# Kernel optimization log

Measured on AMD Instinct MI355X. Metric: run time of the kernel, lower is better.

Reference implementation:

```python
import jax, jax.numpy as jnp
import numpy as np

N, E = 50000, 1600000
DIM_IN, DIM_H, HEADS, DIM_OUT, EDGE_DIM = 64, 16, 8, 64, 1
HID = DIM_H * HEADS  # 128


def setup_inputs() -> dict:
    key = jax.random.key(0)
    ks = jax.random.split(key, 20)
    s = 0.1
    return {
        "x": jax.random.normal(ks[0], (N, DIM_IN), jnp.float32),
        "edge_index": jax.random.randint(ks[1], (2, E), 0, N, jnp.int32),
        "edge_weight": jax.random.uniform(ks[2], (E, EDGE_DIM), jnp.float32),
        # gat1 params (GATv2Conv: lin_l, lin_r with bias, lin_edge no bias, att, out bias)
        "w1_l": jax.random.normal(ks[3], (DIM_IN, HID), jnp.float32) * s,
        "b1_l": jnp.zeros((HID,), jnp.float32),
        "w1_r": jax.random.normal(ks[4], (DIM_IN, HID), jnp.float32) * s,
        "b1_r": jnp.zeros((HID,), jnp.float32),
        "w1_e": jax.random.normal(ks[5], (EDGE_DIM, HID), jnp.float32) * s,
        "att1": jax.random.normal(ks[6], (HEADS, DIM_H), jnp.float32) * s,
        "bias1": jnp.zeros((HID,), jnp.float32),
        # gat2 params (heads=1)
        "w2_l": jax.random.normal(ks[7], (HID, DIM_OUT), jnp.float32) * s,
        "b2_l": jnp.zeros((DIM_OUT,), jnp.float32),
        "w2_r": jax.random.normal(ks[8], (HID, DIM_OUT), jnp.float32) * s,
        "b2_r": jnp.zeros((DIM_OUT,), jnp.float32),
        "w2_e": jax.random.normal(ks[9], (EDGE_DIM, DIM_OUT), jnp.float32) * s,
        "att2": jax.random.normal(ks[10], (1, DIM_OUT), jnp.float32) * s,
        "bias2": jnp.zeros((DIM_OUT,), jnp.float32),
        # final fc
        "fc_w": jax.random.normal(ks[11], (DIM_OUT, 1), jnp.float32) * s,
        "fc_b": jnp.zeros((1,), jnp.float32),
    }


def _gatv2(x, src, dst, eattr, wl, bl, wr, br, we, att, bias, H, C):
    n = x.shape[0]
    xl = (x @ wl + bl).reshape(n, H, C)
    xr = (x @ wr + br).reshape(n, H, C)
    e = (eattr @ we).reshape(-1, H, C)
    # GATv2: score on summed, leaky-relu'd features (edge-wise)
    m = jax.nn.leaky_relu(xl[src] + xr[dst] + e, 0.2)  # [Etot, H, C]
    logits = jnp.einsum('ehc,hc->eh', m, att)
    lmax = jax.ops.segment_max(logits, dst, num_segments=n)
    ex = jnp.exp(logits - lmax[dst])
    denom = jax.ops.segment_sum(ex, dst, num_segments=n)
    alpha = ex / denom[dst]  # segment softmax over neighborhoods
    out = jax.ops.segment_sum(alpha[:, :, None] * xl[src], dst, num_segments=n)
    return out.reshape(n, H * C) + bias


def reference(x, edge_index, edge_weight,
              w1_l, b1_l, w1_r, b1_r, w1_e, att1, bias1,
              w2_l, b2_l, w2_r, b2_r, w2_e, att2, bias2,
              fc_w, fc_b):
    n = x.shape[0]
    src, dst = edge_index[0], edge_index[1]
    # add self-loops with edge_attr fill_value='mean' (PyG default)
    ones = jnp.ones((src.shape[0], 1), x.dtype)
    cnt = jax.ops.segment_sum(ones, dst, num_segments=n)
    sm = jax.ops.segment_sum(edge_weight, dst, num_segments=n)
    mean_attr = jnp.where(cnt > 0, sm / jnp.maximum(cnt, 1.0), 0.0)
    loop = jnp.arange(n, dtype=src.dtype)
    src_f = jnp.concatenate([src, loop])
    dst_f = jnp.concatenate([dst, loop])
    eattr = jnp.concatenate([edge_weight, mean_attr], axis=0)

    # dropout(p=0.6) is identity in eval mode
    h = _gatv2(x, src_f, dst_f, eattr, w1_l, b1_l, w1_r, b1_r, w1_e, att1, bias1, HEADS, DIM_H)
    h = jax.nn.elu(h)
    h = _gatv2(h, src_f, dst_f, eattr, w2_l, b2_l, w2_r, b2_r, w2_e, att2, bias2, 1, DIM_OUT)
    h = jax.nn.log_softmax(h, axis=1)
    return h @ fc_w + fc_b  # [N, 1]
```

## Files before the change

### kernel.cpp

```cpp
#include <hip/hip_runtime.h>
#include <hip/hip_fp16.h>

#define HEADS 8
#define HID 128
#define DIN 64
#define DOUT 64
#define NBLK 512
#define BSH 8
#define BS 256
#define MAXNB 512

typedef _Float16 f16x2 __attribute__((ext_vector_type(2)));
union U8 { uint4 u4[2]; f16x2 h[8]; };
union X8 { uint4 u4[8]; f16x2 h[32]; };

__device__ __forceinline__ int h2i(f16x2 h) { union { f16x2 h; int i; } u; u.h = h; return u.i; }
__device__ __forceinline__ f16x2 i2h(int i) { union { f16x2 h; int i; } u; u.i = i; return u.h; }
__device__ __forceinline__ _Float16 us2h(unsigned short v) { union { unsigned short u; _Float16 h; } u; u.u = v; return u.h; }

__device__ __forceinline__ void cvt16(const uint4 v, f16x2* o) {
#if __has_builtin(__builtin_amdgcn_cvt_scalef32_pk_f16_fp8)
    o[0] = __builtin_amdgcn_cvt_scalef32_pk_f16_fp8(v.x, 1.0f, false);
    o[1] = __builtin_amdgcn_cvt_scalef32_pk_f16_fp8(v.x, 1.0f, true);
    o[2] = __builtin_amdgcn_cvt_scalef32_pk_f16_fp8(v.y, 1.0f, false);
    o[3] = __builtin_amdgcn_cvt_scalef32_pk_f16_fp8(v.y, 1.0f, true);
    o[4] = __builtin_amdgcn_cvt_scalef32_pk_f16_fp8(v.z, 1.0f, false);
    o[5] = __builtin_amdgcn_cvt_scalef32_pk_f16_fp8(v.z, 1.0f, true);
    o[6] = __builtin_amdgcn_cvt_scalef32_pk_f16_fp8(v.w, 1.0f, false);
    o[7] = __builtin_amdgcn_cvt_scalef32_pk_f16_fp8(v.w, 1.0f, true);
#else
    const f16x2 s256 = (f16x2){(_Float16)256.f, (_Float16)256.f};
    const unsigned* uu = &v.x;
#pragma unroll
    for (int j = 0; j < 4; ++j) {
        unsigned u = uu[j];
        unsigned plo = u & 0xFFFFu, phi = u >> 16;
        unsigned flo = ((plo & 0x80u) << 8) | ((plo & 0x7Fu) << 7)
                     | ((plo & 0x8000u) << 16) | ((plo & 0x7F00u) << 15);
        unsigned fhi = ((phi & 0x80u) << 8) | ((phi & 0x7Fu) << 7)
                     | ((phi & 0x8000u) << 16) | ((phi & 0x7F00u) << 15);
        o[2*j]   = i2h((int)flo) * s256;
        o[2*j+1] = i2h((int)fhi) * s256;
    }
#endif
}

__device__ __forceinline__ unsigned enc_fp8(float a) {
    float c = fminf(fmaxf(a, -448.f), 448.f);
    unsigned short hb = __half_as_ushort(__float2half(c));
    unsigned s = ((unsigned)hb >> 8) & 0x80u;
    unsigned lsb = (hb >> 7) & 1u;
    unsigned hr = (unsigned)hb + 0x3Fu + lsb;
    int e = (int)((hr >> 10) & 0x1Fu);
    if (e <= 8) {
        int m8 = (int)rintf(fabsf(c) * 512.f);
        if (m8 >= 8) return s | (1u << 3);
        return s | (unsigned)m8;
    }
    unsigned m3 = (hr >> 7) & 7u;
    int ef = e - 8;
    if (ef > 15) { ef = 15; m3 = 7u; }
    return s | ((unsigned)ef << 3) | m3;
}

__device__ __forceinline__ unsigned char to_fp8(float a) {
#if __has_builtin(__builtin_amdgcn_cvt_pk_fp8_f32)
    int v = __builtin_amdgcn_cvt_pk_fp8_f32(a, a, 0, false);
    return (unsigned char)(v & 0xFF);
#else
    return (unsigned char)enc_fp8(a);
#endif
}

__global__ void k_hist(const int* __restrict__ ei, int* __restrict__ h, int E, int NB) {
    __shared__ int hist[MAXNB];
    int i = blockIdx.x, t = threadIdx.x;
    for (int b = t; b < NB; b += 256) hist[b] = 0;
    __syncthreads();
    int chunk = (E + NBLK - 1) / NBLK;
    int e0 = i * chunk, e1 = min(E, e0 + chunk);
    for (int e = e0 + t; e < e1; e += 256) {
        int d = ei[E + e];
        atomicAdd(&hist[d >> BSH], 1);
    }
    __syncthreads();
    for (int b = t; b < NB; b += 256) h[b * NBLK + i] = hist[b];
}

__global__ void k_scancol(int* __restrict__ h, int* __restrict__ Btot, int NB) {
    __shared__ int s[256];
    int b = blockIdx.x, t = threadIdx.x;
    int* col = h + (size_t)b * NBLK;
    int v0 = col[2 * t], v1 = col[2 * t + 1];
    int pair = v0 + v1;
    s[t] = pair;
    __syncthreads();
    for (int off = 1; off < 256; off <<= 1) {
        int u = (t >= off) ? s[t - off] : 0;
        __syncthreads();
        s[t] += u;
        __syncthreads();
    }
    int excl = s[t] - pair;
    col[2 * t] = excl;
    col[2 * t + 1] = excl + v0;
    if (t == 255) Btot[b] = s[255];
}

__global__ void k_scanbuck(const int* __restrict__ Btot, int* __restrict__ Boff,
                           int* __restrict__ rowptr, int E, int N, int NB) {
    __shared__ int s[256];
    int t = threadIdx.x;
    int v = (t < NB) ? Btot[t] : 0;
    s[t] = v;
    __syncthreads();
    for (int off = 1; off < 256; off <<= 1) {
        int u = (t >= off) ? s[t - off] : 0;
        __syncthreads();
        s[t] += u;
        __syncthreads();
    }
    if (t < NB) Boff[t] = s[t] - v;
    if (t == 0) { Boff[NB] = E; rowptr[N] = E + N; }
}

__global__ void k_scatter(const int* __restrict__ ei, const float* __restrict__ ew,
                          const int* __restrict__ h, const int* __restrict__ Boff,
                          int2* __restrict__ barr, int E, int NB) {
    __shared__ int base[MAXNB];
    int i = blockIdx.x, t = threadIdx.x;
    for (int b = t; b < NB; b += 256) base[b] = h[b * NBLK + i] + Boff[b];
    __syncthreads();
    int chunk = (E + NBLK - 1) / NBLK;
    int e0 = i * chunk, e1 = min(E, e0 + chunk);
    for (int e = e0 + t; e < e1; e += 256) {
        int s = ei[e], d = ei[E + e];
        float w = ew[e];
        int slot = atomicAdd(&base[d >> BSH], 1);
        barr[slot] = make_int2(((d & (BS - 1)) << 16) | s, __float_as_int(w));
    }
}

__global__ void k_csr(const int2* __restrict__ barr, const int* __restrict__ Boff,
                      int* __restrict__ rowptr, unsigned* __restrict__ csrw, int N, int NB) {
    __shared__ int cnt[BS];
    __shared__ int wfix[BS];
    __shared__ int off[BS];
    __shared__ int fill[BS];
    int b = blockIdx.x, t = threadIdx.x;
    int n0 = b << BSH;
    int nodes = min(BS, N - n0);
    cnt[t] = 0; wfix[t] = 0;
    __syncthreads();
    int j0 = Boff[b], j1 = Boff[b + 1];
    for (int j = j0 + t; j < j1; j += BS) {
        int2 rec = barr[j];
        int dl = rec.x >> 16;
        atomicAdd(&cnt[dl], 1);
        atomicAdd(&wfix[dl], (int)(__int_as_float(rec.y) * 16777216.0f));
    }
    __syncthreads();
    int v = (t < nodes) ? cnt[t] + 1 : 0;
    off[t] = v;
    __syncthreads();
    for (int o = 1; o < BS; o <<= 1) {
        int u = (t >= o) ? off[t - o] : 0;
        __syncthreads();
        off[t] += u;
        __syncthreads();
    }
    int rowBase = j0 + n0;
    int rs = rowBase + off[t] - v;
    if (t < nodes) {
        rowptr[n0 + t] = rs;
        int c = cnt[t];
        float mean = (c > 0) ? ((float)wfix[t] * (1.f / 16777216.f)) / (float)c : 0.f;
        csrw[rs + c] = (unsigned)(n0 + t)
                     | ((unsigned)__half_as_ushort(__float2half(mean)) << 16);
        fill[t] = rs;
    }
    __syncthreads();
    for (int j = j0 + t; j < j1; j += BS) {
        int2 rec = barr[j];
        int dl = rec.x >> 16;
        int pos = atomicAdd(&fill[dl], 1);
        unsigned wb = (unsigned)__half_as_ushort(__float2half(__int_as_float(rec.y)));
        csrw[pos] = (unsigned)(rec.x & 0xFFFF) | (wb << 16);
    }
}

__global__ void k_x16(const float* __restrict__ x, __half* __restrict__ x16, int total8) {
    int i = blockIdx.x * blockDim.x + threadIdx.x;
    if (i >= total8) return;
    const float4* p = (const float4*)(x + (size_t)i * 8);
    float4 a = p[0], b = p[1];
    union { __half h[8]; uint4 u; } o;
    o.h[0] = __float2half(a.x); o.h[1] = __float2half(a.y);
    o.h[2] = __float2half(a.z); o.h[3] = __float2half(a.w);
    o.h[4] = __float2half(b.x); o.h[5] = __float2half(b.y);
    o.h[6] = __float2half(b.z); o.h[7] = __float2half(b.w);
    ((uint4*)x16)[i] = o.u;
}

__global__ __launch_bounds__(256) void k_proj1(
        const __half* __restrict__ x16,
        const float* __restrict__ wl, const float* __restrict__ bl,
        const float* __restrict__ wr, const float* __restrict__ br,
        unsigned char* __restrict__ xl8, __half* __restrict__ xr16, int N) {
    int t = threadIdx.x;
    bool isL = t < 128;
    int j = isL ? t : t - 128;
    const float* w = isL ? wl : wr;
    float bj = isL ? bl[j] : br[j];
    f16x2 wreg[32];
#pragma unroll
    for (int k = 0; k < 32; ++k)
        wreg[k] = (f16x2){(_Float16)w[(2*k) * HID + j], (_Float16)w[(2*k+1) * HID + j]};
    for (int n = blockIdx.x; n < N; n += gridDim.x) {
        X8 xa;
        const uint4* xp = (const uint4*)(x16 + (size_t)n * DIN);
#pragma unroll
        for (int q = 0; q < 8; ++q) xa.u4[q] = xp[q];
        float acc = 0.f;
#pragma unroll
        for (int k = 0; k < 32; ++k) acc = __builtin_amdgcn_fdot2(xa.h[k], wreg[k], acc, false);
        acc += bj;
        if (isL) xl8[(size_t)n * HID + j] = to_fp8(acc);
        else     xr16[(size_t)n * HID + j] = __float2half(acc);
    }
}

__global__ __launch_bounds__(128) void k_proj2(
        const __half* __restrict__ h1,
        const float* __restrict__ wl, const float* __restrict__ bl,
        const float* __restrict__ wr, const float* __restrict__ br,
        unsigned char* __restrict__ xl8, __half* __restrict__ xr16, int N) {
    int t = threadIdx.x;
    bool isL = t < 64;
    int j = isL ? t : t - 64;
    const float* w = isL ? wl : wr;
    float bj = isL ? bl[j] : br[j];
    f16x2 wreg0[32], wreg1[32];
#pragma unroll
    for (int k = 0; k < 32; ++k) {
        wreg0[k] = (f16x2){(_Float16)w[(2*k) * DOUT + j], (_Float16)w[(2*k+1) * DOUT + j]};
        wreg1[k] = (f16x2){(_Float16)w[(64 + 2*k) * DOUT + j], (_Float16)w[(64 + 2*k+1) * DOUT + j]};
    }
    for (int n = blockIdx.x; n < N; n += gridDim.x) {
        const uint4* xp = (const uint4*)(h1 + (size_t)n * HID);
        float acc = 0.f;
        {
            X8 xa;
#pragma unroll
            for (int q = 0; q < 8; ++q) xa.u4[q] = xp[q];
#pragma unroll
            for (int k = 0; k < 32; ++k) acc = __builtin_amdgcn_fdot2(xa.h[k], wreg0[k], acc, false);
        }
        {
            X8 xa;
#pragma unroll
            for (int q = 0; q < 8; ++q) xa.u4[q] = xp[8 + q];
#pragma unroll
            for (int k = 0; k < 32; ++k) acc = __builtin_amdgcn_fdot2(xa.h[k], wreg1[k], acc, false);
        }
        acc += bj;
        if (isL) xl8[(size_t)n * DOUT + j] = to_fp8(acc);
        else     xr16[(size_t)n * DOUT + j] = __float2half(acc);
    }
}

#define G1_FETCH(R, SLOT) \
    rec##R = __shfl(creg, (SLOT) * 8 + es); \
    buf##R = *(const uint4*)(xl8 + ((rec##R & 0xFFFFu) * 128u + (unsigned)cb));

#define G1_COMP(R, SLOT) { \
    f16x2 xv[8]; \
    cvt16(buf##R, xv); \
    bool live = (s0 + (SLOT) * 8 + es) < r1; \
    _Float16 wh = us2h((unsigned short)(rec##R >> 16)); \
    f16x2 w2 = (f16x2){wh, wh}; \
    float p0 = 0.f, p1 = 0.f; \
    _Pragma("unroll") \
    for (int k = 0; k < 8; k += 2) { \
        f16x2 m0 = xv[k] + __builtin_elementwise_fma(w2, we2[k], xr.h[k]); \
        m0 = __builtin_elementwise_max(m0, m0 * c02); \
        p0 = __builtin_amdgcn_fdot2(m0, at2[k], p0, false); \
        f16x2 m1 = xv[k+1] + __builtin_elementwise_fma(w2, we2[k+1], xr.h[k+1]); \
        m1 = __builtin_elementwise_max(m1, m1 * c02); \
        p1 = __builtin_amdgcn_fdot2(m1, at2[k+1], p1, false); \
    } \
    float ex = live ? __expf(p0 + p1) : 0.f; \
    den += ex; \
    _Float16 exh = (_Float16)ex; \
    f16x2 ex2 = (f16x2){exh, exh}; \
    _Pragma("unroll") \
    for (int k = 0; k < 8; ++k) num2[k] = __builtin_elementwise_fma(ex2, xv[k], num2[k]); }

__global__ __launch_bounds__(256) void k_gat1(
        const int* __restrict__ rowptr, const unsigned* __restrict__ csr,
        const unsigned char* __restrict__ xl8, const __half* __restrict__ xr16,
        const float* __restrict__ w1e, const float* __restrict__ att,
        const float* __restrict__ bias, __half* __restrict__ h1,
        int N, int totWaves) {
    int lane = threadIdx.x & 63;
    int wv = (blockIdx.x * blockDim.x + threadIdx.x) >> 6;
    int es = lane & 7, h = lane >> 3;
    int cb = h * 16;
    f16x2 we2[8], at2[8];
#pragma unroll
    for (int k = 0; k < 8; ++k) {
        we2[k] = (f16x2){(_Float16)w1e[cb + 2*k], (_Float16)w1e[cb + 2*k + 1]};
        at2[k] = (f16x2){(_Float16)att[cb + 2*k], (_Float16)att[cb + 2*k + 1]};
    }
    float2 bs = *(const float2*)(bias + cb + es * 2);
    const f16x2 c02 = (f16x2){(_Float16)0.2f, (_Float16)0.2f};

    int r0 = 0, r1 = 0;
    if (wv < N) { r0 = rowptr[wv]; r1 = rowptr[wv + 1]; }
    for (int n = wv; n < N; n += totWaves) {
        int nn = n + totWaves;
        int r0n = 0, r1n = 0;
        if (nn < N) { r0n = rowptr[nn]; r1n = rowptr[nn + 1]; }

        U8 xr;
        { const uint4* p = (const uint4*)(xr16 + (unsigned)(n * HID + cb)); xr.u4[0] = p[0]; xr.u4[1] = p[1]; }
        float den = 0.f;
        f16x2 num2[8];
#pragma unroll
        for (int k = 0; k < 8; ++k) num2[k] = (f16x2){(_Float16)0.f, (_Float16)0.f};

        for (int s0 = r0; s0 < r1; s0 += 64) {
            unsigned creg = csr[min(s0 + lane, r1 - 1)];
            unsigned recA, recB, recC;
            uint4 bufA, bufB, bufC;
            G1_FETCH(A, 0)
            G1_FETCH(B, 1)
            G1_FETCH(C, 2)
            G1_COMP(A, 0)
            if (s0 + 24 < r1) { G1_FETCH(A, 3) }
            if (s0 + 8 < r1) {
                G1_COMP(B, 1)
                if (s0 + 32 < r1) { G1_FETCH(B, 4) }
                if (s0 + 16 < r1) {
                    G1_COMP(C, 2)
                    if (s0 + 40 < r1) { G1_FETCH(C, 5) }
                    if (s0 + 24 < r1) {
                        G1_COMP(A, 3)
                        if (s0 + 48 < r1) { G1_FETCH(A, 6) }
                        if (s0 + 32 < r1) {
                            G1_COMP(B, 4)
                            if (s0 + 56 < r1) { G1_FETCH(B, 7) }
                            if (s0 + 40 < r1) {
                                G1_COMP(C, 5)
                                if (s0 + 48 < r1) {
                                    G1_COMP(A, 6)
                                    if (s0 + 56 < r1) {
                                        G1_COMP(B, 7)
                                    }
                                }
                            }
                        }
                    }
                }
            }
        }
        den += __shfl_xor(den, 1); den += __shfl_xor(den, 2); den += __shfl_xor(den, 4);
        bool h4 = es & 4, h2 = es & 2, h1b = es & 1;
        f16x2 r4[4];
#pragma unroll
        for (int k = 0; k < 4; ++k) {
            f16x2 send_ = h4 ? num2[k] : num2[k + 4];
            f16x2 recv = i2h(__shfl_xor(h2i(send_), 4));
            r4[k] = (h4 ? num2[k + 4] : num2[k]) + recv;
        }
        f16x2 r2[2];
#pragma unroll
        for (int k = 0; k < 2; ++k) {
            f16x2 send_ = h2 ? r4[k] : r4[k + 2];
            f16x2 recv = i2h(__shfl_xor(h2i(send_), 2));
            r2[k] = (h2 ? r4[k + 2] : r4[k]) + recv;
        }
        f16x2 send_ = h1b ? r2[0] : r2[1];
        f16x2 recv = i2h(__shfl_xor(h2i(send_), 1));
        f16x2 rfin = (h1b ? r2[1] : r2[0]) + recv;

        float inv = 1.f / den;
        float v0 = fmaf((float)rfin[0], inv, bs.x);
        float v1 = fmaf((float)rfin[1], inv, bs.y);
        v0 = v0 > 0.f ? v0 : expm1f(v0);
        v1 = v1 > 0.f ? v1 : expm1f(v1);
        *(__half2*)(h1 + (unsigned)(n * HID + cb + es * 2)) = __floats2half2_rn(v0, v1);
        r0 = r0n; r1 = r1n;
    }
}

#define G2_FETCH(R, SLOT) \
    rec##R = __shfl(creg, (SLOT) * 16 + es); \
    buf##R = *(const uint4*)(xl8 + ((rec##R & 0xFFFFu) * 64u + (unsigned)cb));

#define G2_COMP(R, SLOT) { \
    f16x2 xv[8]; \
    cvt16(buf##R, xv); \
    bool live = (s0 + (SLOT) * 16 + es) < r1; \
    _Float16 wh = us2h((unsigned short)(rec##R >> 16)); \
    f16x2 w2 = (f16x2){wh, wh}; \
    float p0 = 0.f, p1 = 0.f; \
    _Pragma("unroll") \
    for (int k = 0; k < 8; k += 2) { \
        f16x2 m0 = xv[k] + __builtin_elementwise_fma(w2, we2[k], xr.h[k]); \
        m0 = __builtin_elementwise_max(m0, m0 * c02); \
        p0 = __builtin_amdgcn_fdot2(m0, at2[k], p0, false); \
        f16x2 m1 = xv[k+1] + __builtin_elementwise_fma(w2, we2[k+1], xr.h[k+1]); \
        m1 = __builtin_elementwise_max(m1, m1 * c02); \
        p1 = __builtin_amdgcn_fdot2(m1, at2[k+1], p1, false); \
    } \
    float p = p0 + p1; \
    p += __shfl_xor(p, 1); \
    p += __shfl_xor(p, 2); \
    float ex = live ? __expf(p) : 0.f; \
    den += ex; \
    _Float16 exh = (_Float16)ex; \
    f16x2 ex2 = (f16x2){exh, exh}; \
    _Pragma("unroll") \
    for (int k = 0; k < 8; ++k) num2[k] = __builtin_elementwise_fma(ex2, xv[k], num2[k]); }

__global__ __launch_bounds__(256) void k_gat2(
        const int* __restrict__ rowptr, const unsigned* __restrict__ csr,
        const unsigned char* __restrict__ xl8, const __half* __restrict__ xr16,
        const float* __restrict__ w2e, const float* __restrict__ att,
        const float* __restrict__ bias2, const float* __restrict__ fcw,
        const float* __restrict__ fcb, float* __restrict__ out,
        int N, int totWaves) {
    int lane = threadIdx.x & 63;
    int wv = (blockIdx.x * blockDim.x + threadIdx.x) >> 6;
    int q4 = lane & 3, es = lane >> 2;
    int cb = q4 * 16;
    int cown = cb + es;
    f16x2 we2[8], at2[8];
#pragma unroll
    for (int k = 0; k < 8; ++k) {
        we2[k] = (f16x2){(_Float16)w2e[cb + 2*k], (_Float16)w2e[cb + 2*k + 1]};
        at2[k] = (f16x2){(_Float16)att[cb + 2*k], (_Float16)att[cb + 2*k + 1]};
    }
    float bso = bias2[cown], fcwo = fcw[cown], fcb0 = fcb[0];
    const f16x2 c02 = (f16x2){(_Float16)0.2f, (_Float16)0.2f};

    int r0 = 0, r1 = 0;
    if (wv < N) { r0 = rowptr[wv]; r1 = rowptr[wv + 1]; }
    for (int n = wv; n < N; n += totWaves) {
        int nn = n + totWaves;
        int r0n = 0, r1n = 0;
        if (nn < N) { r0n = rowptr[nn]; r1n = rowptr[nn + 1]; }

        U8 xr;
        { const uint4* p = (const uint4*)(xr16 + (unsigned)(n * DOUT + cb)); xr.u4[0] = p[0]; xr.u4[1] = p[1]; }
        float den = 0.f;
        f16x2 num2[8];
#pragma unroll
        for (int k = 0; k < 8; ++k) num2[k] = (f16x2){(_Float16)0.f, (_Float16)0.f};

        for (int s0 = r0; s0 < r1; s0 += 64) {
            unsigned creg = csr[min(s0 + lane, r1 - 1)];
            unsigned recA, recB, recC;
            uint4 bufA, bufB, bufC;
            G2_FETCH(A, 0)
            G2_FETCH(B, 1)
            G2_FETCH(C, 2)
            G2_COMP(A, 0)
            if (s0 + 48 < r1) { G2_FETCH(A, 3) }
            if (s0 + 16 < r1) {
                G2_COMP(B, 1)
                if (s0 + 32 < r1) {
                    G2_COMP(C, 2)
                    if (s0 + 48 < r1) {
                        G2_COMP(A, 3)
                    }
                }
            }
        }
        den += __shfl_xor(den, 4); den += __shfl_xor(den, 8);
        den += __shfl_xor(den, 16); den += __shfl_xor(den, 32);
        bool b8 = es & 8, b4 = es & 4, b2 = es & 2;
        f16x2 r4[4];
#pragma unroll
        for (int k = 0; k < 4; ++k) {
            f16x2 send_ = b8 ? num2[k] : num2[k + 4];
            f16x2 recv = i2h(__shfl_xor(h2i(send_), 32));
            r4[k] = (b8 ? num2[k + 4] : num2[k]) + recv;
        }
        f16x2 r2[2];
#pragma unroll
        for (int k = 0; k < 2; ++k) {
            f16x2 send_ = b4 ? r4[k] : r4[k + 2];
            f16x2 recv = i2h(__shfl_xor(h2i(send_), 16));
            r2[k] = (b4 ? r4[k + 2] : r4[k]) + recv;
        }
        f16x2 send1 = b2 ? r2[0] : r2[1];
        f16x2 recv1 = i2h(__shfl_xor(h2i(send1), 8));
        f16x2 r1v = (b2 ? r2[1] : r2[0]) + recv1;
        f16x2 rsum = r1v + i2h(__shfl_xor(h2i(r1v), 4));
        float o = (es & 1) ? (float)rsum[1] : (float)rsum[0];
        o = fmaf(o, 1.f / den, bso);
        float mx = o;
#pragma unroll
        for (int off = 1; off < 64; off <<= 1) mx = fmaxf(mx, __shfl_xor(mx, off));
        float exv = __expf(o - mx);
        float ssum = exv;
#pragma unroll
        for (int off = 1; off < 64; off <<= 1) ssum += __shfl_xor(ssum, off);
        float ls = o - mx - __logf(ssum);
        float contrib = ls * fcwo;
#pragma unroll
        for (int off = 1; off < 64; off <<= 1) contrib += __shfl_xor(contrib, off);
        if (lane == 0) out[n] = contrib + fcb0;
        r0 = r0n; r1 = r1n;
    }
}

extern "C" void kernel_launch(void* const* d_in, const int* in_sizes, int n_in,
                              void* d_out, int out_size, void* d_ws, size_t ws_size,
                              hipStream_t stream) {
    const float* x     = (const float*)d_in[0];
    const int*   ei    = (const int*)d_in[1];
    const float* ew    = (const float*)d_in[2];
    const float* w1l   = (const float*)d_in[3];
    const float* b1l   = (const float*)d_in[4];
    const float* w1r   = (const float*)d_in[5];
    const float* b1r   = (const float*)d_in[6];
    const float* w1e   = (const float*)d_in[7];
    const float* att1  = (const float*)d_in[8];
    const float* bias1 = (const float*)d_in[9];
    const float* w2l   = (const float*)d_in[10];
    const float* b2l   = (const float*)d_in[11];
    const float* w2r   = (const float*)d_in[12];
    const float* b2r   = (const float*)d_in[13];
    const float* w2e   = (const float*)d_in[14];
    const float* att2  = (const float*)d_in[15];
    const float* bias2 = (const float*)d_in[16];
    const float* fcw   = (const float*)d_in[17];
    const float* fcb   = (const float*)d_in[18];
    float* out = (float*)d_out;

    int N = in_sizes[0] / DIN;
    int E = in_sizes[1] / 2;
    int Etot = E + N;
    int NB = (N + BS - 1) >> BSH;

    char* base = (char*)d_ws;
    size_t off = 0;
    auto alloc = [&](size_t bytes) -> void* {
        void* p = base + off;
        off += (bytes + 15) & ~(size_t)15;
        return p;
    };
    int*      rowptr = (int*)alloc(((size_t)N + 1) * 4);
    unsigned* csr    = (unsigned*)alloc((size_t)Etot * 4);
    int*      h      = (int*)alloc((size_t)NB * NBLK * 4);
    int*      Btot   = (int*)alloc((size_t)NB * 4);
    int*      Boff   = (int*)alloc(((size_t)NB + 1) * 4);
    char* R = (char*)alloc((size_t)N * HID * 3);
    int2*          barr = (int2*)R;
    unsigned char* xl8  = (unsigned char*)R;
    __half*        xr16 = (__half*)(R + (size_t)N * HID * 1);
    __half*        h1   = (__half*)alloc((size_t)N * HID * 2);
    __half*        x16  = (__half*)alloc((size_t)N * DIN * 2);
    (void)ws_size;

    k_hist<<<NBLK, 256, 0, stream>>>(ei, h, E, NB);
    k_scancol<<<NB, 256, 0, stream>>>(h, Btot, NB);
    k_scanbuck<<<1, 256, 0, stream>>>(Btot, Boff, rowptr, E, N, NB);
    k_scatter<<<NBLK, 256, 0, stream>>>(ei, ew, h, Boff, barr, E, NB);
    k_csr<<<NB, 256, 0, stream>>>(barr, Boff, rowptr, csr, N, NB);

    int tot8 = N * DIN / 8;
    k_x16<<<(tot8 + 255) / 256, 256, 0, stream>>>(x, x16, tot8);

    const int GB = 2048, TB = 256;
    int totWaves = GB * (TB / 64);

    k_proj1<<<2048, 256, 0, stream>>>(x16, w1l, b1l, w1r, b1r, xl8, xr16, N);
    k_gat1<<<GB, TB, 0, stream>>>(rowptr, csr, xl8, xr16, w1e, att1, bias1, h1, N, totWaves);

    k_proj2<<<2048, 128, 0, stream>>>(h1, w2l, b2l, w2r, b2r, xl8, xr16, N);
    k_gat2<<<GB, TB, 0, stream>>>(rowptr, csr, xl8, xr16, w2e, att2, bias2, fcw, fcb, out, N, totWaves);
}
```

Baseline: 211.2 us.

## Process two nodes per wave in GAT1 and widen CSR build blocks

k_gat1 now splits each 64-lane wave into two 32-lane halves that each aggregate a different destination node, with 4 edge slots per head instead of 8. The edge loop runs up to the larger of the two degrees and uses a flattened prefetch chain over 16 slots. This is meant to raise lane utilisation for nodes whose degree is near the average of about 33, where a full 64-edge chunk leaves many lanes idle. In exchange it adds imbalance when the two paired degrees differ and runs more sequential slots per lane. k_csr also moves to 512 threads per block so more threads stream the bucket records.

```diff
diff --git a/kernel.cpp b/kernel.cpp
--- a/kernel.cpp
+++ b/kernel.cpp
@@ -141,8 +141,9 @@
     }
 }
 
-__global__ void k_csr(const int2* __restrict__ barr, const int* __restrict__ Boff,
-                      int* __restrict__ rowptr, unsigned* __restrict__ csrw, int N, int NB) {
+__global__ __launch_bounds__(512) void k_csr(
+        const int2* __restrict__ barr, const int* __restrict__ Boff,
+        int* __restrict__ rowptr, unsigned* __restrict__ csrw, int N, int NB) {
     __shared__ int cnt[BS];
     __shared__ int wfix[BS];
     __shared__ int off[BS];
@@ -150,28 +151,32 @@
     int b = blockIdx.x, t = threadIdx.x;
     int n0 = b << BSH;
     int nodes = min(BS, N - n0);
-    cnt[t] = 0; wfix[t] = 0;
+    if (t < BS) { cnt[t] = 0; wfix[t] = 0; }
     __syncthreads();
     int j0 = Boff[b], j1 = Boff[b + 1];
-    for (int j = j0 + t; j < j1; j += BS) {
+    for (int j = j0 + t; j < j1; j += 512) {
         int2 rec = barr[j];
         int dl = rec.x >> 16;
         atomicAdd(&cnt[dl], 1);
         atomicAdd(&wfix[dl], (int)(__int_as_float(rec.y) * 16777216.0f));
     }
     __syncthreads();
-    int v = (t < nodes) ? cnt[t] + 1 : 0;
-    off[t] = v;
+    int v = 0;
+    if (t < BS) {
+        v = (t < nodes) ? cnt[t] + 1 : 0;
+        off[t] = v;
+    }
     __syncthreads();
     for (int o = 1; o < BS; o <<= 1) {
-        int u = (t >= o) ? off[t - o] : 0;
+        int u = 0;
+        if (t < BS && t >= o) u = off[t - o];
         __syncthreads();
-        off[t] += u;
+        if (t < BS) off[t] += u;
         __syncthreads();
     }
     int rowBase = j0 + n0;
-    int rs = rowBase + off[t] - v;
     if (t < nodes) {
+        int rs = rowBase + off[t] - v;
         rowptr[n0 + t] = rs;
         int c = cnt[t];
         float mean = (c > 0) ? ((float)wfix[t] * (1.f / 16777216.f)) / (float)c : 0.f;
@@ -180,7 +185,7 @@
         fill[t] = rs;
     }
     __syncthreads();
-    for (int j = j0 + t; j < j1; j += BS) {
+    for (int j = j0 + t; j < j1; j += 512) {
         int2 rec = barr[j];
         int dl = rec.x >> 16;
         int pos = atomicAdd(&fill[dl], 1);
@@ -270,13 +275,13 @@
 }
 
 #define G1_FETCH(R, SLOT) \
-    rec##R = __shfl(creg, (SLOT) * 8 + es); \
+    rec##R = __shfl(((SLOT) < 8 ? creg0 : creg1), (lane & 32) | (((SLOT) & 7) * 4 + es)); \
     buf##R = *(const uint4*)(xl8 + ((rec##R & 0xFFFFu) * 128u + (unsigned)cb));
 
 #define G1_COMP(R, SLOT) { \
     f16x2 xv[8]; \
     cvt16(buf##R, xv); \
-    bool live = (s0 + (SLOT) * 8 + es) < r1; \
+    bool live = (crel + (SLOT) * 4 + es) < d; \
     _Float16 wh = us2h((unsigned short)(rec##R >> 16)); \
     f16x2 w2 = (f16x2){wh, wh}; \
     float p0 = 0.f, p1 = 0.f; \
@@ -304,23 +309,28 @@
         int N, int totWaves) {
     int lane = threadIdx.x & 63;
     int wv = (blockIdx.x * blockDim.x + threadIdx.x) >> 6;
-    int es = lane & 7, h = lane >> 3;
-    int cb = h * 16;
+    int half = lane >> 5;
+    int hl = lane & 31;
+    int es = hl & 3, hd = hl >> 2;
+    int cb = hd * 16;
     f16x2 we2[8], at2[8];
 #pragma unroll
     for (int k = 0; k < 8; ++k) {
         we2[k] = (f16x2){(_Float16)w1e[cb + 2*k], (_Float16)w1e[cb + 2*k + 1]};
         at2[k] = (f16x2){(_Float16)att[cb + 2*k], (_Float16)att[cb + 2*k + 1]};
     }
-    float2 bs = *(const float2*)(bias + cb + es * 2);
+    float4 bs4 = *(const float4*)(bias + cb + es * 4);
     const f16x2 c02 = (f16x2){(_Float16)0.2f, (_Float16)0.2f};
 
-    int r0 = 0, r1 = 0;
-    if (wv < N) { r0 = rowptr[wv]; r1 = rowptr[wv + 1]; }
-    for (int n = wv; n < N; n += totWaves) {
-        int nn = n + totWaves;
-        int r0n = 0, r1n = 0;
-        if (nn < N) { r0n = rowptr[nn]; r1n = rowptr[nn + 1]; }
+    int pstride = totWaves * 2;
+    int pn0 = wv * 2;
+    int r0 = 0, r1 = 1;
+    if (pn0 < N) { int n = pn0 + half; r0 = rowptr[n]; r1 = rowptr[n + 1]; }
+    for (int pn = pn0; pn < N; pn += pstride) {
+        int n = pn + half;
+        int pnn = pn + pstride;
+        int r0n = 0, r1n = 1;
+        if (pnn < N) { int nn = pnn + half; r0n = rowptr[nn]; r1n = rowptr[nn + 1]; }
 
         U8 xr;
         { const uint4* p = (const uint4*)(xr16 + (unsigned)(n * HID + cb)); xr.u4[0] = p[0]; xr.u4[1] = p[1]; }
@@ -329,67 +339,64 @@
 #pragma unroll
         for (int k = 0; k < 8; ++k) num2[k] = (f16x2){(_Float16)0.f, (_Float16)0.f};
 
-        for (int s0 = r0; s0 < r1; s0 += 64) {
-            unsigned creg = csr[min(s0 + lane, r1 - 1)];
+        int d = r1 - r0;
+        int dmax = max(d, __shfl_xor(d, 32));
+        int r1m1 = r1 - 1;
+
+        for (int crel = 0; crel < dmax; crel += 64) {
+            unsigned creg0 = csr[min(r0 + crel + hl, r1m1)];
+            unsigned creg1 = csr[min(r0 + crel + 32 + hl, r1m1)];
             unsigned recA, recB, recC;
             uint4 bufA, bufB, bufC;
             G1_FETCH(A, 0)
             G1_FETCH(B, 1)
             G1_FETCH(C, 2)
-            G1_COMP(A, 0)
-            if (s0 + 24 < r1) { G1_FETCH(A, 3) }
-            if (s0 + 8 < r1) {
-                G1_COMP(B, 1)
-                if (s0 + 32 < r1) { G1_FETCH(B, 4) }
-                if (s0 + 16 < r1) {
-                    G1_COMP(C, 2)
-                    if (s0 + 40 < r1) { G1_FETCH(C, 5) }
-                    if (s0 + 24 < r1) {
-                        G1_COMP(A, 3)
-                        if (s0 + 48 < r1) { G1_FETCH(A, 6) }
-                        if (s0 + 32 < r1) {
-                            G1_COMP(B, 4)
-                            if (s0 + 56 < r1) { G1_FETCH(B, 7) }
-                            if (s0 + 40 < r1) {
-                                G1_COMP(C, 5)
-                                if (s0 + 48 < r1) {
-                                    G1_COMP(A, 6)
-                                    if (s0 + 56 < r1) {
-                                        G1_COMP(B, 7)
-                                    }
-                                }
-                            }
-                        }
-                    }
-                }
-            }
-        }
-        den += __shfl_xor(den, 1); den += __shfl_xor(den, 2); den += __shfl_xor(den, 4);
-        bool h4 = es & 4, h2 = es & 2, h1b = es & 1;
+            G1_COMP(A, 0)  if (crel + 12 < dmax) { G1_FETCH(A, 3) }
+            if (crel + 4  < dmax) { G1_COMP(B, 1)  if (crel + 16 < dmax) { G1_FETCH(B, 4) } }
+            if (crel + 8  < dmax) { G1_COMP(C, 2)  if (crel + 20 < dmax) { G1_FETCH(C, 5) } }
+            if (crel + 12 < dmax) { G1_COMP(A, 3)  if (crel + 24 < dmax) { G1_FETCH(A, 6) } }
+            if (crel + 16 < dmax) { G1_COMP(B, 4)  if (crel + 28 < dmax) { G1_FETCH(B, 7) } }
+            if (crel + 20 < dmax) { G1_COMP(C, 5)  if (crel + 32 < dmax) { G1_FETCH(C, 8) } }
+            if (crel + 24 < dmax) { G1_COMP(A, 6)  if (crel + 36 < dmax) { G1_FETCH(A, 9) } }
+            if (crel + 28 < dmax) { G1_COMP(B, 7)  if (crel + 40 < dmax) { G1_FETCH(B, 10) } }
+            if (crel + 32 < dmax) { G1_COMP(C, 8)  if (crel + 44 < dmax) { G1_FETCH(C, 11) } }
+            if (crel + 36 < dmax) { G1_COMP(A, 9)  if (crel + 48 < dmax) { G1_FETCH(A, 12) } }
+            if (crel + 40 < dmax) { G1_COMP(B, 10) if (crel + 52 < dmax) { G1_FETCH(B, 13) } }
+            if (crel + 44 < dmax) { G1_COMP(C, 11) if (crel + 56 < dmax) { G1_FETCH(C, 14) } }
+            if (crel + 48 < dmax) { G1_COMP(A, 12) if (crel + 60 < dmax) { G1_FETCH(A, 15) } }
+            if (crel + 52 < dmax) { G1_COMP(B, 13) }
+            if (crel + 56 < dmax) { G1_COMP(C, 14) }
+            if (crel + 60 < dmax) { G1_COMP(A, 15) }
+        }
+        den += __shfl_xor(den, 1); den += __shfl_xor(den, 2);
+        bool e2 = es & 2, e1 = es & 1;
         f16x2 r4[4];
 #pragma unroll
         for (int k = 0; k < 4; ++k) {
-            f16x2 send_ = h4 ? num2[k] : num2[k + 4];
-            f16x2 recv = i2h(__shfl_xor(h2i(send_), 4));
-            r4[k] = (h4 ? num2[k + 4] : num2[k]) + recv;
+            f16x2 send_ = e2 ? num2[k] : num2[k + 4];
+            f16x2 recv = i2h(__shfl_xor(h2i(send_), 2));
+            r4[k] = (e2 ? num2[k + 4] : num2[k]) + recv;
         }
         f16x2 r2[2];
 #pragma unroll
         for (int k = 0; k < 2; ++k) {
-            f16x2 send_ = h2 ? r4[k] : r4[k + 2];
-            f16x2 recv = i2h(__shfl_xor(h2i(send_), 2));
-            r2[k] = (h2 ? r4[k + 2] : r4[k]) + recv;
-        }
-        f16x2 send_ = h1b ? r2[0] : r2[1];
-        f16x2 recv = i2h(__shfl_xor(h2i(send_), 1));
-        f16x2 rfin = (h1b ? r2[1] : r2[0]) + recv;
-
+            f16x2 send_ = e1 ? r4[k] : r4[k + 2];
+            f16x2 recv = i2h(__shfl_xor(h2i(send_), 1));
+            r2[k] = (e1 ? r4[k + 2] : r4[k]) + recv;
+        }
         float inv = 1.f / den;
-        float v0 = fmaf((float)rfin[0], inv, bs.x);
-        float v1 = fmaf((float)rfin[1], inv, bs.y);
+        float v0 = fmaf((float)r2[0][0], inv, bs4.x);
+        float v1 = fmaf((float)r2[0][1], inv, bs4.y);
+        float v2 = fmaf((float)r2[1][0], inv, bs4.z);
+        float v3 = fmaf((float)r2[1][1], inv, bs4.w);
         v0 = v0 > 0.f ? v0 : expm1f(v0);
         v1 = v1 > 0.f ? v1 : expm1f(v1);
-        *(__half2*)(h1 + (unsigned)(n * HID + cb + es * 2)) = __floats2half2_rn(v0, v1);
+        v2 = v2 > 0.f ? v2 : expm1f(v2);
+        v3 = v3 > 0.f ? v3 : expm1f(v3);
+        union { __half2 h2[2]; uint2 u; } st;
+        st.h2[0] = __floats2half2_rn(v0, v1);
+        st.h2[1] = __floats2half2_rn(v2, v3);
+        *(uint2*)(h1 + (unsigned)(n * HID + cb + es * 4)) = st.u;
         r0 = r0n; r1 = r1n;
     }
 }
@@ -570,7 +577,7 @@
     k_scancol<<<NB, 256, 0, stream>>>(h, Btot, NB);
     k_scanbuck<<<1, 256, 0, stream>>>(Btot, Boff, rowptr, E, N, NB);
     k_scatter<<<NBLK, 256, 0, stream>>>(ei, ew, h, Boff, barr, E, NB);
-    k_csr<<<NB, 256, 0, stream>>>(barr, Boff, rowptr, csr, N, NB);
+    k_csr<<<NB, 512, 0, stream>>>(barr, Boff, rowptr, csr, N, NB);
 
     int tot8 = N * DIN / 8;
     k_x16<<<(tot8 + 255) / 256, 256, 0, stream>>>(x, x16, tot8);
```

After: 206.4 us, median of 2. 1.02x faster.

## Split GAT layer-1 aggregation into two head-half passes with separate fp8 tables

Applied to the files above, without the earlier changes.

Layer-1 source features are now stored as two separate 64-byte-per-node fp8 tables, one per half of the heads. The aggregation kernel runs twice, once per half, with each lane group handling 16 edges at a time. The intent is to halve the working set of random gathers so each pass's table fits better in cache, at the cost of reading the CSR twice and launching an extra kernel. The CSR build kernel also moves to 512 threads per block to speed up the edge loops.

```diff
diff --git a/kernel.cpp b/kernel.cpp
--- a/kernel.cpp
+++ b/kernel.cpp
@@ -141,8 +141,9 @@
     }
 }
 
-__global__ void k_csr(const int2* __restrict__ barr, const int* __restrict__ Boff,
-                      int* __restrict__ rowptr, unsigned* __restrict__ csrw, int N, int NB) {
+__global__ __launch_bounds__(512) void k_csr(
+        const int2* __restrict__ barr, const int* __restrict__ Boff,
+        int* __restrict__ rowptr, unsigned* __restrict__ csrw, int N, int NB) {
     __shared__ int cnt[BS];
     __shared__ int wfix[BS];
     __shared__ int off[BS];
@@ -150,28 +151,32 @@
     int b = blockIdx.x, t = threadIdx.x;
     int n0 = b << BSH;
     int nodes = min(BS, N - n0);
-    cnt[t] = 0; wfix[t] = 0;
+    if (t < BS) { cnt[t] = 0; wfix[t] = 0; }
     __syncthreads();
     int j0 = Boff[b], j1 = Boff[b + 1];
-    for (int j = j0 + t; j < j1; j += BS) {
+    for (int j = j0 + t; j < j1; j += 512) {
         int2 rec = barr[j];
         int dl = rec.x >> 16;
         atomicAdd(&cnt[dl], 1);
         atomicAdd(&wfix[dl], (int)(__int_as_float(rec.y) * 16777216.0f));
     }
     __syncthreads();
-    int v = (t < nodes) ? cnt[t] + 1 : 0;
-    off[t] = v;
+    int v = 0;
+    if (t < BS) {
+        v = (t < nodes) ? cnt[t] + 1 : 0;
+        off[t] = v;
+    }
     __syncthreads();
     for (int o = 1; o < BS; o <<= 1) {
-        int u = (t >= o) ? off[t - o] : 0;
+        int u = 0;
+        if (t < BS && t >= o) u = off[t - o];
         __syncthreads();
-        off[t] += u;
+        if (t < BS) off[t] += u;
         __syncthreads();
     }
     int rowBase = j0 + n0;
-    int rs = rowBase + off[t] - v;
     if (t < nodes) {
+        int rs = rowBase + off[t] - v;
         rowptr[n0 + t] = rs;
         int c = cnt[t];
         float mean = (c > 0) ? ((float)wfix[t] * (1.f / 16777216.f)) / (float)c : 0.f;
@@ -180,7 +185,7 @@
         fill[t] = rs;
     }
     __syncthreads();
-    for (int j = j0 + t; j < j1; j += BS) {
+    for (int j = j0 + t; j < j1; j += 512) {
         int2 rec = barr[j];
         int dl = rec.x >> 16;
         int pos = atomicAdd(&fill[dl], 1);
@@ -206,7 +211,8 @@
         const __half* __restrict__ x16,
         const float* __restrict__ wl, const float* __restrict__ bl,
         const float* __restrict__ wr, const float* __restrict__ br,
-        unsigned char* __restrict__ xl8, __half* __restrict__ xr16, int N) {
+        unsigned char* __restrict__ xl8a, unsigned char* __restrict__ xl8b,
+        __half* __restrict__ xr16, int N) {
     int t = threadIdx.x;
     bool isL = t < 128;
     int j = isL ? t : t - 128;
@@ -216,6 +222,8 @@
 #pragma unroll
     for (int k = 0; k < 32; ++k)
         wreg[k] = (f16x2){(_Float16)w[(2*k) * HID + j], (_Float16)w[(2*k+1) * HID + j]};
+    unsigned char* xl8p = (j < 64) ? xl8a : xl8b;
+    int jc = j & 63;
     for (int n = blockIdx.x; n < N; n += gridDim.x) {
         X8 xa;
         const uint4* xp = (const uint4*)(x16 + (size_t)n * DIN);
@@ -225,7 +233,7 @@
 #pragma unroll
         for (int k = 0; k < 32; ++k) acc = __builtin_amdgcn_fdot2(xa.h[k], wreg[k], acc, false);
         acc += bj;
-        if (isL) xl8[(size_t)n * HID + j] = to_fp8(acc);
+        if (isL) xl8p[(size_t)n * 64 + jc] = to_fp8(acc);
         else     xr16[(size_t)n * HID + j] = __float2half(acc);
     }
 }
@@ -269,14 +277,14 @@
     }
 }
 
-#define G1_FETCH(R, SLOT) \
-    rec##R = __shfl(creg, (SLOT) * 8 + es); \
-    buf##R = *(const uint4*)(xl8 + ((rec##R & 0xFFFFu) * 128u + (unsigned)cb));
-
-#define G1_COMP(R, SLOT) { \
+#define GP_FETCH(R, SLOT) \
+    rec##R = __shfl(creg, (SLOT) * 16 + es); \
+    buf##R = *(const uint4*)(xl8p + ((rec##R & 0xFFFFu) * 64u + (unsigned)cb));
+
+#define GP_COMP(R, SLOT) { \
     f16x2 xv[8]; \
     cvt16(buf##R, xv); \
-    bool live = (s0 + (SLOT) * 8 + es) < r1; \
+    bool live = (s0 + (SLOT) * 16 + es) < r1; \
     _Float16 wh = us2h((unsigned short)(rec##R >> 16)); \
     f16x2 w2 = (f16x2){wh, wh}; \
     float p0 = 0.f, p1 = 0.f; \
@@ -296,23 +304,24 @@
     _Pragma("unroll") \
     for (int k = 0; k < 8; ++k) num2[k] = __builtin_elementwise_fma(ex2, xv[k], num2[k]); }
 
-__global__ __launch_bounds__(256) void k_gat1(
+__global__ __launch_bounds__(256) void k_gat1p(
         const int* __restrict__ rowptr, const unsigned* __restrict__ csr,
-        const unsigned char* __restrict__ xl8, const __half* __restrict__ xr16,
+        const unsigned char* __restrict__ xl8p, const __half* __restrict__ xr16,
         const float* __restrict__ w1e, const float* __restrict__ att,
         const float* __restrict__ bias, __half* __restrict__ h1,
-        int N, int totWaves) {
+        int N, int totWaves, int po) {
     int lane = threadIdx.x & 63;
     int wv = (blockIdx.x * blockDim.x + threadIdx.x) >> 6;
-    int es = lane & 7, h = lane >> 3;
-    int cb = h * 16;
+    int q4 = lane & 3, es = lane >> 2;
+    int cb = q4 * 16;
+    int cown = cb + es;
     f16x2 we2[8], at2[8];
 #pragma unroll
     for (int k = 0; k < 8; ++k) {
-        we2[k] = (f16x2){(_Float16)w1e[cb + 2*k], (_Float16)w1e[cb + 2*k + 1]};
-        at2[k] = (f16x2){(_Float16)att[cb + 2*k], (_Float16)att[cb + 2*k + 1]};
-    }
-    float2 bs = *(const float2*)(bias + cb + es * 2);
+        we2[k] = (f16x2){(_Float16)w1e[po + cb + 2*k], (_Float16)w1e[po + cb + 2*k + 1]};
+        at2[k] = (f16x2){(_Float16)att[po + cb + 2*k], (_Float16)att[po + cb + 2*k + 1]};
+    }
+    float bso = bias[po + cown];
     const f16x2 c02 = (f16x2){(_Float16)0.2f, (_Float16)0.2f};
 
     int r0 = 0, r1 = 0;
@@ -323,7 +332,7 @@
         if (nn < N) { r0n = rowptr[nn]; r1n = rowptr[nn + 1]; }
 
         U8 xr;
-        { const uint4* p = (const uint4*)(xr16 + (unsigned)(n * HID + cb)); xr.u4[0] = p[0]; xr.u4[1] = p[1]; }
+        { const uint4* p = (const uint4*)(xr16 + (unsigned)(n * HID + po + cb)); xr.u4[0] = p[0]; xr.u4[1] = p[1]; }
         float den = 0.f;
         f16x2 num2[8];
 #pragma unroll
@@ -333,63 +342,46 @@
             unsigned creg = csr[min(s0 + lane, r1 - 1)];
             unsigned recA, recB, recC;
             uint4 bufA, bufB, bufC;
-            G1_FETCH(A, 0)
-            G1_FETCH(B, 1)
-            G1_FETCH(C, 2)
-            G1_COMP(A, 0)
-            if (s0 + 24 < r1) { G1_FETCH(A, 3) }
-            if (s0 + 8 < r1) {
-                G1_COMP(B, 1)
-                if (s0 + 32 < r1) { G1_FETCH(B, 4) }
-                if (s0 + 16 < r1) {
-                    G1_COMP(C, 2)
-                    if (s0 + 40 < r1) { G1_FETCH(C, 5) }
-                    if (s0 + 24 < r1) {
-                        G1_COMP(A, 3)
-                        if (s0 + 48 < r1) { G1_FETCH(A, 6) }
-                        if (s0 + 32 < r1) {
-                            G1_COMP(B, 4)
-                            if (s0 + 56 < r1) { G1_FETCH(B, 7) }
-                            if (s0 + 40 < r1) {
-                                G1_COMP(C, 5)
-                                if (s0 + 48 < r1) {
-                                    G1_COMP(A, 6)
-                                    if (s0 + 56 < r1) {
-                                        G1_COMP(B, 7)
-                                    }
-                                }
-                            }
-                        }
+            GP_FETCH(A, 0)
+            GP_FETCH(B, 1)
+            GP_FETCH(C, 2)
+            GP_COMP(A, 0)
+            if (s0 + 48 < r1) { GP_FETCH(A, 3) }
+            if (s0 + 16 < r1) {
+                GP_COMP(B, 1)
+                if (s0 + 32 < r1) {
+                    GP_COMP(C, 2)
+                    if (s0 + 48 < r1) {
+                        GP_COMP(A, 3)
                     }
                 }
             }
         }
-        den += __shfl_xor(den, 1); den += __shfl_xor(den, 2); den += __shfl_xor(den, 4);
-        bool h4 = es & 4, h2 = es & 2, h1b = es & 1;
+        den += __shfl_xor(den, 4); den += __shfl_xor(den, 8);
+        den += __shfl_xor(den, 16); den += __shfl_xor(den, 32);
+        bool b8 = es & 8, b4 = es & 4, b2 = es & 2;
         f16x2 r4[4];
 #pragma unroll
         for (int k = 0; k < 4; ++k) {
-            f16x2 send_ = h4 ? num2[k] : num2[k + 4];
-            f16x2 recv = i2h(__shfl_xor(h2i(send_), 4));
-            r4[k] = (h4 ? num2[k + 4] : num2[k]) + recv;
+            f16x2 send_ = b8 ? num2[k] : num2[k + 4];
+            f16x2 recv = i2h(__shfl_xor(h2i(send_), 32));
+            r4[k] = (b8 ? num2[k + 4] : num2[k]) + recv;
         }
         f16x2 r2[2];
 #pragma unroll
         for (int k = 0; k < 2; ++k) {
-            f16x2 send_ = h2 ? r4[k] : r4[k + 2];
-            f16x2 recv = i2h(__shfl_xor(h2i(send_), 2));
-            r2[k] = (h2 ? r4[k + 2] : r4[k]) + recv;
-        }
-        f16x2 send_ = h1b ? r2[0] : r2[1];
-        f16x2 recv = i2h(__shfl_xor(h2i(send_), 1));
-        f16x2 rfin = (h1b ? r2[1] : r2[0]) + recv;
-
-        float inv = 1.f / den;
-        float v0 = fmaf((float)rfin[0], inv, bs.x);
-        float v1 = fmaf((float)rfin[1], inv, bs.y);
-        v0 = v0 > 0.f ? v0 : expm1f(v0);
-        v1 = v1 > 0.f ? v1 : expm1f(v1);
-        *(__half2*)(h1 + (unsigned)(n * HID + cb + es * 2)) = __floats2half2_rn(v0, v1);
+            f16x2 send_ = b4 ? r4[k] : r4[k + 2];
+            f16x2 recv = i2h(__shfl_xor(h2i(send_), 16));
+            r2[k] = (b4 ? r4[k + 2] : r4[k]) + recv;
+        }
+        f16x2 send1 = b2 ? r2[0] : r2[1];
+        f16x2 recv1 = i2h(__shfl_xor(h2i(send1), 8));
+        f16x2 r1v = (b2 ? r2[1] : r2[0]) + recv1;
+        f16x2 rsum = r1v + i2h(__shfl_xor(h2i(r1v), 4));
+        float o = (es & 1) ? (float)rsum[1] : (float)rsum[0];
+        float v = fmaf(o, 1.f / den, bso);
+        v = v > 0.f ? v : expm1f(v);
+        h1[(unsigned)(n * HID + po + cown)] = __float2half(v);
         r0 = r0n; r1 = r1n;
     }
 }
@@ -560,7 +552,8 @@
     int*      Boff   = (int*)alloc(((size_t)NB + 1) * 4);
     char* R = (char*)alloc((size_t)N * HID * 3);
     int2*          barr = (int2*)R;
-    unsigned char* xl8  = (unsigned char*)R;
+    unsigned char* xl8a = (unsigned char*)R;
+    unsigned char* xl8b = (unsigned char*)(R + (size_t)N * 64);
     __half*        xr16 = (__half*)(R + (size_t)N * HID * 1);
     __half*        h1   = (__half*)alloc((size_t)N * HID * 2);
     __half*        x16  = (__half*)alloc((size_t)N * DIN * 2);
@@ -570,7 +563,7 @@
     k_scancol<<<NB, 256, 0, stream>>>(h, Btot, NB);
     k_scanbuck<<<1, 256, 0, stream>>>(Btot, Boff, rowptr, E, N, NB);
     k_scatter<<<NBLK, 256, 0, stream>>>(ei, ew, h, Boff, barr, E, NB);
-    k_csr<<<NB, 256, 0, stream>>>(barr, Boff, rowptr, csr, N, NB);
+    k_csr<<<NB, 512, 0, stream>>>(barr, Boff, rowptr, csr, N, NB);
 
     int tot8 = N * DIN / 8;
     k_x16<<<(tot8 + 255) / 256, 256, 0, stream>>>(x, x16, tot8);
@@ -578,9 +571,10 @@
     const int GB = 2048, TB = 256;
     int totWaves = GB * (TB / 64);
 
-    k_proj1<<<2048, 256, 0, stream>>>(x16, w1l, b1l, w1r, b1r, xl8, xr16, N);
-    k_gat1<<<GB, TB, 0, stream>>>(rowptr, csr, xl8, xr16, w1e, att1, bias1, h1, N, totWaves);
-
-    k_proj2<<<2048, 128, 0, stream>>>(h1, w2l, b2l, w2r, b2r, xl8, xr16, N);
-    k_gat2<<<GB, TB, 0, stream>>>(rowptr, csr, xl8, xr16, w2e, att2, bias2, fcw, fcb, out, N, totWaves);
-}
+    k_proj1<<<2048, 256, 0, stream>>>(x16, w1l, b1l, w1r, b1r, xl8a, xl8b, xr16, N);
+    k_gat1p<<<GB, TB, 0, stream>>>(rowptr, csr, xl8a, xr16, w1e, att1, bias1, h1, N, totWaves, 0);
+    k_gat1p<<<GB, TB, 0, stream>>>(rowptr, csr, xl8b, xr16, w1e, att1, bias1, h1, N, totWaves, 64);
+
+    k_proj2<<<2048, 128, 0, stream>>>(h1, w2l, b2l, w2r, b2r, xl8a, xr16, N);
+    k_gat2<<<GB, TB, 0, stream>>>(rowptr, csr, xl8a, xr16, w2e, att2, bias2, fcw, fcb, out, N, totWaves);
+}
```

Result: slower. 227.1 us (+7.6%).
